# Performance work log

Measured on AMD Instinct MI355X. Metric: run time of the kernel, lower is better.

Reference implementation:

```python
import jax, jax.numpy as jnp
import numpy as np

N = 50000
E = 800000
IN_DIM = 256
HID = 64
HEADS = 4
OUT_DIM = 40
NEG_SLOPE = 0.2


def _gatv2_conv(x, src, dst, Wl, bl, Wr, br, att, bias, concat):
    """PyG GATv2Conv (share_weights=False, eval mode, no attn dropout).
    src -> message source nodes, dst -> target nodes (softmax over dst)."""
    H, C = att.shape
    n = x.shape[0]
    xl = (x @ Wl + bl).reshape(n, H, C)  # source/message transform (lin_l)
    xr = (x @ Wr + br).reshape(n, H, C)  # target transform (lin_r)
    # per-edge logits: [E, H]
    s = xl[src] + xr[dst]                                  # [E,H,C]
    e = jnp.einsum('ehc,hc->eh', jax.nn.leaky_relu(s, NEG_SLOPE), att)
    # segment softmax over incoming edges of each target node
    m = jax.ops.segment_max(e, dst, num_segments=n)        # [N,H]
    m = jnp.where(jnp.isfinite(m), m, 0.0)                 # empty segments
    ex = jnp.exp(e - m[dst])
    denom = jax.ops.segment_sum(ex, dst, num_segments=n)   # [N,H]
    alpha = ex / (denom[dst] + 1e-16)                      # [E,H]
    out = jax.ops.segment_sum(alpha[:, :, None] * xl[src], dst, num_segments=n)
    if concat:
        out = out.reshape(n, H * C)
    else:
        out = out.mean(axis=1)
    return out + bias


def setup_inputs() -> dict:
    key = jax.random.key(0)
    ks = jax.random.split(key, 12)
    sc = 0.05
    return {
        'x': jax.random.normal(ks[0], (N, IN_DIM), jnp.float32),
        'src': jax.random.randint(ks[1], (E,), 0, N, jnp.int32),
        'dst': jax.random.randint(ks[2], (E,), 0, N, jnp.int32),
        'Wl1': jax.random.normal(ks[3], (IN_DIM, HEADS * HID), jnp.float32) * sc,
        'bl1': jnp.zeros((HEADS * HID,), jnp.float32),
        'Wr1': jax.random.normal(ks[4], (IN_DIM, HEADS * HID), jnp.float32) * sc,
        'br1': jnp.zeros((HEADS * HID,), jnp.float32),
        'att1': jax.random.normal(ks[5], (HEADS, HID), jnp.float32) * sc,
        'bias1': jnp.zeros((HEADS * HID,), jnp.float32),
        'Wl2': jax.random.normal(ks[6], (HEADS * HID, HEADS * HID), jnp.float32) * sc,
        'bl2': jnp.zeros((HEADS * HID,), jnp.float32),
        'Wr2': jax.random.normal(ks[7], (HEADS * HID, HEADS * HID), jnp.float32) * sc,
        'br2': jnp.zeros((HEADS * HID,), jnp.float32),
        'att2': jax.random.normal(ks[8], (HEADS, HID), jnp.float32) * sc,
        'bias2': jnp.zeros((HID,), jnp.float32),
        'Wc': jax.random.normal(ks[9], (HID, OUT_DIM), jnp.float32) * sc,
        'bc': jnp.zeros((OUT_DIM,), jnp.float32),
    }


def reference(x, src, dst, Wl1, bl1, Wr1, br1, att1, bias1,
              Wl2, bl2, Wr2, br2, att2, bias2, Wc, bc):
    h = _gatv2_conv(x, src, dst, Wl1, bl1, Wr1, br1, att1, bias1, concat=True)
    h = jax.nn.relu(h)  # dropout p applied only in training; eval -> identity
    h = _gatv2_conv(h, src, dst, Wl2, bl2, Wr2, br2, att2, bias2, concat=False)
    h = jax.nn.relu(h)
    return h @ Wc + bc  # [N, OUT_DIM]
```

## Files before the change

### kernel.cpp

```cpp
#include <hip/hip_runtime.h>
#include <hip/hip_bf16.h>
#include <math.h>


#define IN_DIM 256
#define HIDHC 256
#define HID 64
#define OUT_DIM 40

using half8  = __attribute__((ext_vector_type(8))) _Float16;
using half4  = __attribute__((ext_vector_type(4))) _Float16;
using half2v = __attribute__((ext_vector_type(2))) _Float16;
using f32x4  = __attribute__((ext_vector_type(4))) float;

__device__ __forceinline__ void gload16(const void* g, void* l) {
    __builtin_amdgcn_global_load_lds(
        (const __attribute__((address_space(1))) void*)g,
        (__attribute__((address_space(3))) void*)l, 16, 0, 0);
}

__global__ void hist_prep(const int* __restrict__ dst, int* __restrict__ deg,
                          int* __restrict__ rank, int E, int nbh,
                          const float* __restrict__ x, _Float16* __restrict__ Af,
                          const float* __restrict__ W0, const float* __restrict__ W1,
                          const float* __restrict__ W2, const float* __restrict__ W3,
                          _Float16* __restrict__ T, int n4, int nb_cvt) {
    int bid = blockIdx.x;
    if (bid < nbh) {
        int i = bid * 256 + threadIdx.x;
        if (i < E) rank[i] = atomicAdd(&deg[dst[i]], 1);
    } else if (bid < nbh + nb_cvt) {
        int i = (bid - nbh) * 256 + threadIdx.x;
        if (i >= n4) return;
        float4 v = ((const float4*)x)[i];
        half4 h = { (_Float16)v.x, (_Float16)v.y, (_Float16)v.z, (_Float16)v.w };
        int node = i >> 6;
        int kb = (i & 63) * 4;
        size_t a = (size_t)(node >> 7) * 32768 + (size_t)(kb >> 3) * 1024
                 + (size_t)(node & 127) * 8 + (kb & 7);
        *(half4*)(Af + a) = h;
    } else {
        int widx = bid - nbh - nb_cvt;
        int wsel = widx >> 8, k = widx & 255, nn = threadIdx.x;
        const float* Wsel = (wsel == 0) ? W0 : (wsel == 1) ? W1
                          : (wsel == 2) ? W2 : W3;
        float v = Wsel[k * 256 + nn];
        size_t a = (size_t)wsel * 65536
                 + (size_t)(nn >> 7) * 32768 + (size_t)(k >> 5) * 4096
                 + (size_t)((k >> 3) & 3) * 1024 + (size_t)(nn & 127) * 8 + (k & 7);
        T[a] = (_Float16)v;
    }
}

__global__ void deg_block_reduce(const int* __restrict__ deg, int* __restrict__ bsum, int n) {
    int i = blockIdx.x * 256 + threadIdx.x;
    int v = (i < n) ? deg[i] : 0;
    #pragma unroll
    for (int off = 32; off; off >>= 1) v += __shfl_xor(v, off, 64);
    __shared__ int ws[4];
    int lane = threadIdx.x & 63, wid = threadIdx.x >> 6;
    if (lane == 0) ws[wid] = v;
    __syncthreads();
    if (threadIdx.x == 0) bsum[blockIdx.x] = ws[0] + ws[1] + ws[2] + ws[3];
}

__global__ void deg_scan_apply(const int* __restrict__ deg, const int* __restrict__ bsum,
                               int* __restrict__ offsets, int n, int nb) {
    int tid = threadIdx.x;
    int lane = tid & 63, wid = tid >> 6;

    __shared__ int pws[4];
    __shared__ int sadd;
    int pv = (tid < nb && tid < (int)blockIdx.x) ? bsum[tid] : 0;
    #pragma unroll
    for (int off = 32; off; off >>= 1) pv += __shfl_xor(pv, off, 64);
    if (lane == 0) pws[wid] = pv;
    __syncthreads();
    if (tid == 0) sadd = pws[0] + pws[1] + pws[2] + pws[3];
    __syncthreads();

    int i = blockIdx.x * 256 + tid;
    int v = (i < n) ? deg[i] : 0;
    int inc = v;
    #pragma unroll
    for (int off = 1; off < 64; off <<= 1) {
        int t = __shfl_up(inc, off, 64);
        if (lane >= off) inc += t;
    }
    __shared__ int ws[4];
    if (lane == 63) ws[wid] = inc;
    __syncthreads();
    int add = sadd;
    for (int w = 0; w < wid; ++w) add += ws[w];
    int incl = inc + add;
    if (i < n) offsets[i + 1] = incl;
    if (i == 0) offsets[0] = 0;
}


__device__ __forceinline__ void gemm_tile(
    const _Float16* __restrict__ Apk,
    const _Float16* __restrict__ W0, const float* __restrict__ b0, _Float16* __restrict__ C0,
    const _Float16* __restrict__ W1, const float* __restrict__ b1, _Float16* __restrict__ C1,
    int M, int bx, int by, _Float16* sA, _Float16* sW)
{
    int tid = threadIdx.x;
    int bm = bx * 128;
    int bn = by * 128;

    int lane = tid & 63, w = tid >> 6;
    int z  = w >> 2, wq = w & 3;
    int r = lane & 15, q = lane >> 4;
    int m0 = (wq >> 1) * 64, n0 = (wq & 1) * 64;

    const _Float16* Abase = Apk + (size_t)bx * 32768;
    const _Float16* W0b   = W0  + (size_t)by * 32768;
    const _Float16* W1b   = W1  + (size_t)by * 32768;
    int go = tid * 8;

    f32x4 acc[4][4];
    #pragma unroll
    for (int i = 0; i < 4; ++i)
        #pragma unroll
        for (int j = 0; j < 4; ++j) acc[i][j] = (f32x4)0.f;

    gload16(Abase + go, sA + go);
    gload16(W0b + go, sW + go);
    gload16(W1b + go, sW + 4096 + go);
    __builtin_amdgcn_s_waitcnt(0);
    __syncthreads();

    #pragma unroll 1
    for (int kt = 0; kt < 8; ++kt) {
        int buf = kt & 1;
        if (kt < 7) {
            int k0 = (kt + 1) * 4096;
            gload16(Abase + k0 + go, sA + (buf ^ 1) * 4096 + go);
            gload16(W0b + k0 + go, sW + ((buf ^ 1) * 2 + 0) * 4096 + go);
            gload16(W1b + k0 + go, sW + ((buf ^ 1) * 2 + 1) * 4096 + go);
        }
        half8 a[4], b[4];
        #pragma unroll
        for (int i = 0; i < 4; ++i) {
            a[i] = *(const half8*)(sA + buf * 4096 + (q * 128 + m0 + i * 16 + r) * 8);
            b[i] = *(const half8*)(sW + (buf * 2 + z) * 4096 + (q * 128 + n0 + i * 16 + r) * 8);
        }
        #pragma unroll
        for (int i = 0; i < 4; ++i)
            #pragma unroll
            for (int j = 0; j < 4; ++j)
                acc[i][j] = __builtin_amdgcn_mfma_f32_16x16x32_f16(a[i], b[j], acc[i][j], 0, 0, 0);
        __builtin_amdgcn_s_waitcnt(0);
        __syncthreads();
    }

    const float* bias = z ? b1 : b0;
    _Float16*    C    = z ? C1 : C0;

    float bv[4];
    #pragma unroll
    for (int j = 0; j < 4; ++j) bv[j] = bias[bn + n0 + j * 16 + r];
    #pragma unroll
    for (int i = 0; i < 4; ++i) {
        #pragma unroll
        for (int reg = 0; reg < 4; ++reg) {
            int orow = bm + m0 + i * 16 + q * 4 + reg;
            if (orow < M) {
                #pragma unroll
                for (int j = 0; j < 4; ++j)
                    C[(size_t)orow * 256 + bn + n0 + j * 16 + r] =
                        (_Float16)(acc[i][j][reg] + bv[j]);
            }
        }
    }
}

__global__ __launch_bounds__(512) void gemm_dual(
    const _Float16* __restrict__ Apk,
    const _Float16* __restrict__ W0, const float* __restrict__ b0, _Float16* __restrict__ C0,
    const _Float16* __restrict__ W1, const float* __restrict__ b1, _Float16* __restrict__ C1,
    int M)
{
    __shared__ __align__(16) _Float16 sA[2 * 4096];
    __shared__ __align__(16) _Float16 sW[2 * 2 * 4096];
    gemm_tile(Apk, W0, b0, C0, W1, b1, C1, M, blockIdx.x, blockIdx.y, sA, sW);
}

__global__ __launch_bounds__(512) void gemm_scatter(
    const _Float16* __restrict__ Apk,
    const _Float16* __restrict__ W0, const float* __restrict__ b0, _Float16* __restrict__ C0,
    const _Float16* __restrict__ W1, const float* __restrict__ b1, _Float16* __restrict__ C1,
    int M, int nbs,
    const int* __restrict__ src, const int* __restrict__ dst,
    const int* __restrict__ rank, const int* __restrict__ offsets,
    int* __restrict__ csr_src, int E)
{
    __shared__ __align__(16) _Float16 sA[2 * 4096];
    __shared__ __align__(16) _Float16 sW[2 * 2 * 4096];
    if ((int)blockIdx.x < nbs) {
        int e = blockIdx.x * 512 + threadIdx.x;
        if (e < E) {
            int d = dst[e];
            csr_src[offsets[d] + rank[e]] = src[e];
        }
        return;
    }
    int g = blockIdx.x - nbs;
    gemm_tile(Apk, W0, b0, C0, W1, b1, C1, M, g >> 1, g & 1, sA, sW);
}


__global__ __launch_bounds__(256) void gat_node(
    const _Float16* __restrict__ xl, const _Float16* __restrict__ xr,
    const float* __restrict__ att, const float* __restrict__ bias,
    const int* __restrict__ offsets, const int* __restrict__ csr_src,
    void* __restrict__ out0, int n, int mode)
{
    int wid = threadIdx.x >> 6;
    int node = (blockIdx.x << 2) + wid;
    if (node >= n) return;
    int lane = threadIdx.x & 63;
    int H = lane >> 5;
    int p = lane & 31;

    const half2v c02 = { (_Float16)0.2f, (_Float16)0.2f };

    half8 xrh = *(const half8*)(xr + (size_t)node * HIDHC + p * 8);
    half2v xr01 = __builtin_shufflevector(xrh, xrh, 0, 1);
    half2v xr23 = __builtin_shufflevector(xrh, xrh, 2, 3);
    half2v xr45 = __builtin_shufflevector(xrh, xrh, 4, 5);
    half2v xr67 = __builtin_shufflevector(xrh, xrh, 6, 7);

    float4 af0 = *(const float4*)(att + p * 8);
    float4 af1 = *(const float4*)(att + p * 8 + 4);
    half2v at01 = { (_Float16)af0.x, (_Float16)af0.y };
    half2v at23 = { (_Float16)af0.z, (_Float16)af0.w };
    half2v at45 = { (_Float16)af1.x, (_Float16)af1.y };
    half2v at67 = { (_Float16)af1.z, (_Float16)af1.w };

    float acc[8];
    #pragma unroll
    for (int k = 0; k < 8; ++k) acc[k] = 0.f;
    float d = 0.f;

    auto edge_compute = [&](half8 h) {
        half2v h01 = __builtin_shufflevector(h, h, 0, 1);
        half2v h23 = __builtin_shufflevector(h, h, 2, 3);
        half2v h45 = __builtin_shufflevector(h, h, 4, 5);
        half2v h67 = __builtin_shufflevector(h, h, 6, 7);
        half2v s01 = h01 + xr01, s23 = h23 + xr23, s45 = h45 + xr45, s67 = h67 + xr67;
        half2v l01 = __builtin_elementwise_max(s01, s01 * c02);
        half2v l23 = __builtin_elementwise_max(s23, s23 * c02);
        half2v l45 = __builtin_elementwise_max(s45, s45 * c02);
        half2v l67 = __builtin_elementwise_max(s67, s67 * c02);
        float e = __builtin_amdgcn_fdot2(l01, at01, 0.f, false);
        e = __builtin_amdgcn_fdot2(l23, at23, e, false);
        e = __builtin_amdgcn_fdot2(l45, at45, e, false);
        e = __builtin_amdgcn_fdot2(l67, at67, e, false);
        e += __shfl_xor(e, 1);
        e += __shfl_xor(e, 2);
        e += __shfl_xor(e, 4);
        float pw = __expf(e);
        d += pw;
        #pragma unroll
        for (int k = 0; k < 8; ++k) acc[k] = fmaf(pw, (float)h[k], acc[k]);
    };

    int j0 = __builtin_amdgcn_readfirstlane(offsets[node]);
    int j1 = __builtin_amdgcn_readfirstlane(offsets[node + 1]);
    int deg = j1 - j0;

    int fast = min(deg, 64);
    int npf = fast >> 1;
    int idxv = 0;
    if (lane < fast) idxv = csr_src[j0 + lane];

    half8 hA, hB;
    if (npf > 0) { int s = __shfl(idxv, 0 + H, 64); hA = *(const half8*)(xl + (size_t)s * HIDHC + p * 8); }
    if (npf > 1) { int s = __shfl(idxv, 2 + H, 64); hB = *(const half8*)(xl + (size_t)s * HIDHC + p * 8); }
    int t = 0;
    for (; t + 4 <= npf; t += 2) {
        half8 ha = hA, hb = hB;
        { int s = __shfl(idxv, (t + 2) * 2 + H, 64); hA = *(const half8*)(xl + (size_t)s * HIDHC + p * 8); }
        { int s = __shfl(idxv, (t + 3) * 2 + H, 64); hB = *(const half8*)(xl + (size_t)s * HIDHC + p * 8); }
        edge_compute(ha);
        edge_compute(hb);
    }
    if (t + 2 <= npf) {
        half8 ha = hA, hb = hB;
        if (t + 2 < npf) { int s = __shfl(idxv, (t + 2) * 2 + H, 64); hA = *(const half8*)(xl + (size_t)s * HIDHC + p * 8); }
        edge_compute(ha);
        edge_compute(hb);
        t += 2;
    }
    if (t < npf) {
        edge_compute(hA);
    }

    int j = j0 + (npf << 1);
    for (; j + 2 <= j1; j += 2) {
        int s0 = __builtin_amdgcn_readfirstlane(csr_src[j]);
        int s1 = __builtin_amdgcn_readfirstlane(csr_src[j + 1]);
        int s = H ? s1 : s0;
        half8 h = *(const half8*)(xl + (size_t)s * HIDHC + p * 8);
        edge_compute(h);
    }
    if (j < j1) {
        int s0 = __builtin_amdgcn_readfirstlane(csr_src[j]);
        half8 h = *(const half8*)(xl + (size_t)s0 * HIDHC + p * 8);
        half2v h01 = __builtin_shufflevector(h, h, 0, 1);
        half2v h23 = __builtin_shufflevector(h, h, 2, 3);
        half2v h45 = __builtin_shufflevector(h, h, 4, 5);
        half2v h67 = __builtin_shufflevector(h, h, 6, 7);
        half2v s01 = h01 + xr01, s23 = h23 + xr23, s45 = h45 + xr45, s67 = h67 + xr67;
        half2v l01 = __builtin_elementwise_max(s01, s01 * c02);
        half2v l23 = __builtin_elementwise_max(s23, s23 * c02);
        half2v l45 = __builtin_elementwise_max(s45, s45 * c02);
        half2v l67 = __builtin_elementwise_max(s67, s67 * c02);
        float e = __builtin_amdgcn_fdot2(l01, at01, 0.f, false);
        e = __builtin_amdgcn_fdot2(l23, at23, e, false);
        e = __builtin_amdgcn_fdot2(l45, at45, e, false);
        e = __builtin_amdgcn_fdot2(l67, at67, e, false);
        e += __shfl_xor(e, 1);
        e += __shfl_xor(e, 2);
        e += __shfl_xor(e, 4);
        float pw = (H == 0) ? __expf(e) : 0.f;
        d += pw;
        #pragma unroll
        for (int k = 0; k < 8; ++k) acc[k] = fmaf(pw, (float)h[k], acc[k]);
    }

    d += __shfl_xor(d, 32);
    #pragma unroll
    for (int k = 0; k < 8; ++k) acc[k] += __shfl_xor(acc[k], 32);

    float inv = 1.f / (d + 1e-16f);
    float o[8];
    #pragma unroll
    for (int k = 0; k < 8; ++k) o[k] = acc[k] * inv;

    if (mode == 0) {
        if (H == 0) {
            float4 b0 = *(const float4*)(bias + p * 8);
            float4 b1 = *(const float4*)(bias + p * 8 + 4);
            float bb[8] = { b0.x, b0.y, b0.z, b0.w, b1.x, b1.y, b1.z, b1.w };
            half8 hh;
            #pragma unroll
            for (int k = 0; k < 8; ++k) hh[k] = (_Float16)fmaxf(o[k] + bb[k], 0.f);
            _Float16* dstp = (_Float16*)out0 + (size_t)(node >> 7) * 32768
                           + (size_t)p * 1024 + (size_t)(node & 127) * 8;
            *(half8*)dstp = hh;
        }
    } else {
        #pragma unroll
        for (int k = 0; k < 8; ++k) {
            o[k] += __shfl_xor(o[k], 8);
            o[k] += __shfl_xor(o[k], 16);
        }
        if (lane < 8) {
            float4 b0 = *(const float4*)(bias + p * 8);
            float4 b1 = *(const float4*)(bias + p * 8 + 4);
            float bb[8] = { b0.x, b0.y, b0.z, b0.w, b1.x, b1.y, b1.z, b1.w };
            float4 o0, o1;
            o0.x = fmaxf(o[0] * 0.25f + bb[0], 0.f);
            o0.y = fmaxf(o[1] * 0.25f + bb[1], 0.f);
            o0.z = fmaxf(o[2] * 0.25f + bb[2], 0.f);
            o0.w = fmaxf(o[3] * 0.25f + bb[3], 0.f);
            o1.x = fmaxf(o[4] * 0.25f + bb[4], 0.f);
            o1.y = fmaxf(o[5] * 0.25f + bb[5], 0.f);
            o1.z = fmaxf(o[6] * 0.25f + bb[6], 0.f);
            o1.w = fmaxf(o[7] * 0.25f + bb[7], 0.f);
            float* dstp = (float*)out0 + (size_t)node * HID + p * 8;
            *(float4*)dstp = o0;
            *(float4*)(dstp + 4) = o1;
        }
    }
}


__global__ __launch_bounds__(256) void final_linear(
    const float* __restrict__ h2, const float* __restrict__ Wc,
    const float* __restrict__ bc, float* __restrict__ out, int n)
{
    __shared__ float Ws[HID * OUT_DIM];
    __shared__ float bs[OUT_DIM];
    __shared__ float hs[64][HID + 1];

    for (int i = threadIdx.x; i < HID * OUT_DIM; i += 256) Ws[i] = Wc[i];
    if (threadIdx.x < OUT_DIM) bs[threadIdx.x] = bc[threadIdx.x];

    int n0 = blockIdx.x * 64;
    for (int i = threadIdx.x; i < 64 * HID; i += 256) {
        int r = i >> 6, c = i & 63;
        int node = n0 + r;
        hs[r][c] = (node < n) ? h2[(size_t)node * HID + c] : 0.f;
    }
    __syncthreads();

    for (int idx = threadIdx.x; idx < 64 * OUT_DIM; idx += 256) {
        int r = idx / OUT_DIM, o = idx % OUT_DIM;
        int node = n0 + r;
        if (node < n) {
            float s = bs[o];
            #pragma unroll
            for (int c = 0; c < HID; ++c) s = fmaf(hs[r][c], Ws[c * OUT_DIM + o], s);
            out[(size_t)node * OUT_DIM + o] = s;
        }
    }
}


extern "C" void kernel_launch(void* const* d_in, const int* in_sizes, int n_in,
                              void* d_out, int out_size, void* d_ws, size_t ws_size,
                              hipStream_t stream) {
    const int N = in_sizes[0] / IN_DIM;
    const int E = in_sizes[1];

    const float* x    = (const float*)d_in[0];
    const int*   src  = (const int*)d_in[1];
    const int*   dst  = (const int*)d_in[2];
    const float* Wl1  = (const float*)d_in[3];
    const float* bl1  = (const float*)d_in[4];
    const float* Wr1  = (const float*)d_in[5];
    const float* br1  = (const float*)d_in[6];
    const float* att1 = (const float*)d_in[7];
    const float* bias1= (const float*)d_in[8];
    const float* Wl2  = (const float*)d_in[9];
    const float* bl2  = (const float*)d_in[10];
    const float* Wr2  = (const float*)d_in[11];
    const float* br2  = (const float*)d_in[12];
    const float* att2 = (const float*)d_in[13];
    const float* bias2= (const float*)d_in[14];
    const float* Wc   = (const float*)d_in[15];
    const float* bc   = (const float*)d_in[16];

    char* ws = (char*)d_ws;
    size_t off = 0;
    const int NT = (N + 127) / 128;
    _Float16* xlh = (_Float16*)(ws + off); off += (size_t)N * HIDHC * 2;
    _Float16* xrh = (_Float16*)(ws + off); off += (size_t)N * HIDHC * 2;
    _Float16* Af  = (_Float16*)(ws + off); off += (size_t)NT * 32768 * 2;
    float*    h2  = (float*)(ws + off);    off += (size_t)N * HID * 4;
    _Float16* Wt  = (_Float16*)(ws + off); off += (size_t)4 * 65536 * 2;
    int* deg     = (int*)(ws + off); off += (size_t)N * 4;
    int* offsets = (int*)(ws + off); off += (size_t)(N + 1) * 4;
    int* rank    = (int*)(ws + off); off += (size_t)E * 4;
    int* csr     = (int*)(ws + off); off += (size_t)E * 4;
    int* bsum    = (int*)(ws + off); off += 256 * 4;

    const int NB = (N + 255) / 256;

    hipMemsetAsync(deg, 0, (size_t)N * 4, stream);
    if (N & 127)
        hipMemsetAsync(Af + (size_t)(NT - 1) * 32768, 0, 32768 * 2, stream);

    const int nbh = (E + 255) / 256;
    const int n4 = N * HIDHC / 4;
    const int nb_cvt = (n4 + 255) / 256;
    hist_prep<<<nbh + nb_cvt + 1024, 256, 0, stream>>>(
        dst, deg, rank, E, nbh, x, Af, Wl1, Wr1, Wl2, Wr2, Wt, n4, nb_cvt);

    deg_block_reduce<<<NB, 256, 0, stream>>>(deg, bsum, N);
    deg_scan_apply<<<NB, 256, 0, stream>>>(deg, bsum, offsets, N, NB);

    const int KW = 65536;
    const int nbs = (E + 511) / 512;
    gemm_scatter<<<nbs + 2 * NT, 512, 0, stream>>>(Af,
        Wt + 0 * KW, bl1, xlh,
        Wt + 1 * KW, br1, xrh, N, nbs,
        src, dst, rank, offsets, csr, E);

    gat_node<<<(N + 3) / 4, 256, 0, stream>>>(xlh, xrh, att1, bias1, offsets, csr,
                                              (void*)Af, N, 0);
    gemm_dual<<<dim3(NT, 2), 512, 0, stream>>>(Af,
        Wt + 2 * KW, bl2, xlh,
        Wt + 3 * KW, br2, xrh, N);
    gat_node<<<(N + 3) / 4, 256, 0, stream>>>(xlh, xrh, att2, bias2, offsets, csr,
                                              (void*)h2, N, 1);
    final_linear<<<(N + 63) / 64, 256, 0, stream>>>(h2, Wc, bc, (float*)d_out, N);
}
```

Baseline: 381.5 us.

## Replace CSR build with fixed 64-slot per-node edge buckets plus overflow list

Builds per-destination adjacency directly during the histogram pass by writing each source into a fixed 64-entry slot array indexed by the atomic rank, with a global overflow list for degrees above 64. This removes the two prefix-scan kernels and the separate scatter pass, so the layer-1 GEMM can run as a plain dual GEMM. The node kernel reads degree and slots directly and scans the whole overflow list for high-degree nodes. The trade-offs are a larger padded CSR buffer with sparser reads, and a linear overflow scan that is slow if many nodes exceed 64 edges. With average degree 16, such nodes should be rare.

After: 386.0 us. About the same (+1.2%).

```diff
diff --git a/kernel.cpp b/kernel.cpp
--- a/kernel.cpp
+++ b/kernel.cpp
@@ -19,16 +19,28 @@
         (__attribute__((address_space(3))) void*)l, 16, 0, 0);
 }
 
-__global__ void hist_prep(const int* __restrict__ dst, int* __restrict__ deg,
-                          int* __restrict__ rank, int E, int nbh,
-                          const float* __restrict__ x, _Float16* __restrict__ Af,
-                          const float* __restrict__ W0, const float* __restrict__ W1,
-                          const float* __restrict__ W2, const float* __restrict__ W3,
-                          _Float16* __restrict__ T, int n4, int nb_cvt) {
+__global__ void hist_csr_prep(const int* __restrict__ src, const int* __restrict__ dst,
+                              int* __restrict__ deg, int* __restrict__ csr,
+                              int* __restrict__ oflow_cnt, int* __restrict__ oflow,
+                              int E, int nbh,
+                              const float* __restrict__ x, _Float16* __restrict__ Af,
+                              const float* __restrict__ W0, const float* __restrict__ W1,
+                              const float* __restrict__ W2, const float* __restrict__ W3,
+                              _Float16* __restrict__ T, int n4, int nb_cvt) {
     int bid = blockIdx.x;
     if (bid < nbh) {
         int i = bid * 256 + threadIdx.x;
-        if (i < E) rank[i] = atomicAdd(&deg[dst[i]], 1);
+        if (i < E) {
+            int d = dst[i];
+            int r = atomicAdd(&deg[d], 1);
+            if (r < 64) {
+                csr[d * 64 + r] = src[i];
+            } else {
+                int q = atomicAdd(oflow_cnt, 1);
+                oflow[2 * q] = d;
+                oflow[2 * q + 1] = src[i];
+            }
+        }
     } else if (bid < nbh + nb_cvt) {
         int i = (bid - nbh) * 256 + threadIdx.x;
         if (i >= n4) return;
@@ -52,51 +64,6 @@
     }
 }
 
-__global__ void deg_block_reduce(const int* __restrict__ deg, int* __restrict__ bsum, int n) {
-    int i = blockIdx.x * 256 + threadIdx.x;
-    int v = (i < n) ? deg[i] : 0;
-    #pragma unroll
-    for (int off = 32; off; off >>= 1) v += __shfl_xor(v, off, 64);
-    __shared__ int ws[4];
-    int lane = threadIdx.x & 63, wid = threadIdx.x >> 6;
-    if (lane == 0) ws[wid] = v;
-    __syncthreads();
-    if (threadIdx.x == 0) bsum[blockIdx.x] = ws[0] + ws[1] + ws[2] + ws[3];
-}
-
-__global__ void deg_scan_apply(const int* __restrict__ deg, const int* __restrict__ bsum,
-                               int* __restrict__ offsets, int n, int nb) {
-    int tid = threadIdx.x;
-    int lane = tid & 63, wid = tid >> 6;
-
-    __shared__ int pws[4];
-    __shared__ int sadd;
-    int pv = (tid < nb && tid < (int)blockIdx.x) ? bsum[tid] : 0;
-    #pragma unroll
-    for (int off = 32; off; off >>= 1) pv += __shfl_xor(pv, off, 64);
-    if (lane == 0) pws[wid] = pv;
-    __syncthreads();
-    if (tid == 0) sadd = pws[0] + pws[1] + pws[2] + pws[3];
-    __syncthreads();
-
-    int i = blockIdx.x * 256 + tid;
-    int v = (i < n) ? deg[i] : 0;
-    int inc = v;
-    #pragma unroll
-    for (int off = 1; off < 64; off <<= 1) {
-        int t = __shfl_up(inc, off, 64);
-        if (lane >= off) inc += t;
-    }
-    __shared__ int ws[4];
-    if (lane == 63) ws[wid] = inc;
-    __syncthreads();
-    int add = sadd;
-    for (int w = 0; w < wid; ++w) add += ws[w];
-    int incl = inc + add;
-    if (i < n) offsets[i + 1] = incl;
-    if (i == 0) offsets[0] = 0;
-}
-
 
 __device__ __forceinline__ void gemm_tile(
     const _Float16* __restrict__ Apk,
@@ -186,34 +153,12 @@
     gemm_tile(Apk, W0, b0, C0, W1, b1, C1, M, blockIdx.x, blockIdx.y, sA, sW);
 }
 
-__global__ __launch_bounds__(512) void gemm_scatter(
-    const _Float16* __restrict__ Apk,
-    const _Float16* __restrict__ W0, const float* __restrict__ b0, _Float16* __restrict__ C0,
-    const _Float16* __restrict__ W1, const float* __restrict__ b1, _Float16* __restrict__ C1,
-    int M, int nbs,
-    const int* __restrict__ src, const int* __restrict__ dst,
-    const int* __restrict__ rank, const int* __restrict__ offsets,
-    int* __restrict__ csr_src, int E)
-{
-    __shared__ __align__(16) _Float16 sA[2 * 4096];
-    __shared__ __align__(16) _Float16 sW[2 * 2 * 4096];
-    if ((int)blockIdx.x < nbs) {
-        int e = blockIdx.x * 512 + threadIdx.x;
-        if (e < E) {
-            int d = dst[e];
-            csr_src[offsets[d] + rank[e]] = src[e];
-        }
-        return;
-    }
-    int g = blockIdx.x - nbs;
-    gemm_tile(Apk, W0, b0, C0, W1, b1, C1, M, g >> 1, g & 1, sA, sW);
-}
-
 
 __global__ __launch_bounds__(256) void gat_node(
     const _Float16* __restrict__ xl, const _Float16* __restrict__ xr,
     const float* __restrict__ att, const float* __restrict__ bias,
-    const int* __restrict__ offsets, const int* __restrict__ csr_src,
+    const int* __restrict__ degv, const int* __restrict__ csr_src,
+    const int* __restrict__ oflow_cnt, const int* __restrict__ oflow,
     void* __restrict__ out0, int n, int mode)
 {
     int wid = threadIdx.x >> 6;
@@ -265,49 +210,7 @@
         #pragma unroll
         for (int k = 0; k < 8; ++k) acc[k] = fmaf(pw, (float)h[k], acc[k]);
     };
-
-    int j0 = __builtin_amdgcn_readfirstlane(offsets[node]);
-    int j1 = __builtin_amdgcn_readfirstlane(offsets[node + 1]);
-    int deg = j1 - j0;
-
-    int fast = min(deg, 64);
-    int npf = fast >> 1;
-    int idxv = 0;
-    if (lane < fast) idxv = csr_src[j0 + lane];
-
-    half8 hA, hB;
-    if (npf > 0) { int s = __shfl(idxv, 0 + H, 64); hA = *(const half8*)(xl + (size_t)s * HIDHC + p * 8); }
-    if (npf > 1) { int s = __shfl(idxv, 2 + H, 64); hB = *(const half8*)(xl + (size_t)s * HIDHC + p * 8); }
-    int t = 0;
-    for (; t + 4 <= npf; t += 2) {
-        half8 ha = hA, hb = hB;
-        { int s = __shfl(idxv, (t + 2) * 2 + H, 64); hA = *(const half8*)(xl + (size_t)s * HIDHC + p * 8); }
-        { int s = __shfl(idxv, (t + 3) * 2 + H, 64); hB = *(const half8*)(xl + (size_t)s * HIDHC + p * 8); }
-        edge_compute(ha);
-        edge_compute(hb);
-    }
-    if (t + 2 <= npf) {
-        half8 ha = hA, hb = hB;
-        if (t + 2 < npf) { int s = __shfl(idxv, (t + 2) * 2 + H, 64); hA = *(const half8*)(xl + (size_t)s * HIDHC + p * 8); }
-        edge_compute(ha);
-        edge_compute(hb);
-        t += 2;
-    }
-    if (t < npf) {
-        edge_compute(hA);
-    }
-
-    int j = j0 + (npf << 1);
-    for (; j + 2 <= j1; j += 2) {
-        int s0 = __builtin_amdgcn_readfirstlane(csr_src[j]);
-        int s1 = __builtin_amdgcn_readfirstlane(csr_src[j + 1]);
-        int s = H ? s1 : s0;
-        half8 h = *(const half8*)(xl + (size_t)s * HIDHC + p * 8);
-        edge_compute(h);
-    }
-    if (j < j1) {
-        int s0 = __builtin_amdgcn_readfirstlane(csr_src[j]);
-        half8 h = *(const half8*)(xl + (size_t)s0 * HIDHC + p * 8);
+    auto edge_compute_single = [&](half8 h) {
         half2v h01 = __builtin_shufflevector(h, h, 0, 1);
         half2v h23 = __builtin_shufflevector(h, h, 2, 3);
         half2v h45 = __builtin_shufflevector(h, h, 4, 5);
@@ -328,6 +231,53 @@
         d += pw;
         #pragma unroll
         for (int k = 0; k < 8; ++k) acc[k] = fmaf(pw, (float)h[k], acc[k]);
+    };
+
+    int dg = __builtin_amdgcn_readfirstlane(degv[node]);
+    int j0 = node << 6;
+
+    int fast = min(dg, 64);
+    int npf = fast >> 1;
+    int idxv = 0;
+    if (lane < fast) idxv = csr_src[j0 + lane];
+
+    half8 hA, hB;
+    if (npf > 0) { int s = __shfl(idxv, 0 + H, 64); hA = *(const half8*)(xl + (size_t)s * HIDHC + p * 8); }
+    if (npf > 1) { int s = __shfl(idxv, 2 + H, 64); hB = *(const half8*)(xl + (size_t)s * HIDHC + p * 8); }
+    int t = 0;
+    for (; t + 4 <= npf; t += 2) {
+        half8 ha = hA, hb = hB;
+        { int s = __shfl(idxv, (t + 2) * 2 + H, 64); hA = *(const half8*)(xl + (size_t)s * HIDHC + p * 8); }
+        { int s = __shfl(idxv, (t + 3) * 2 + H, 64); hB = *(const half8*)(xl + (size_t)s * HIDHC + p * 8); }
+        edge_compute(ha);
+        edge_compute(hb);
+    }
+    if (t + 2 <= npf) {
+        half8 ha = hA, hb = hB;
+        if (t + 2 < npf) { int s = __shfl(idxv, (t + 2) * 2 + H, 64); hA = *(const half8*)(xl + (size_t)s * HIDHC + p * 8); }
+        edge_compute(ha);
+        edge_compute(hb);
+        t += 2;
+    }
+    if (t < npf) {
+        edge_compute(hA);
+    }
+    if (fast & 1) {
+        int s0 = __shfl(idxv, fast - 1, 64);
+        half8 h = *(const half8*)(xl + (size_t)s0 * HIDHC + p * 8);
+        edge_compute_single(h);
+    }
+
+    if (dg > 64) {
+        int cnt = __builtin_amdgcn_readfirstlane(oflow_cnt[0]);
+        for (int k = 0; k < cnt; ++k) {
+            int dd = __builtin_amdgcn_readfirstlane(oflow[2 * k]);
+            if (dd == node) {
+                int ss = __builtin_amdgcn_readfirstlane(oflow[2 * k + 1]);
+                half8 h = *(const half8*)(xl + (size_t)ss * HIDHC + p * 8);
+                edge_compute_single(h);
+            }
+        }
     }
 
     d += __shfl_xor(d, 32);
@@ -442,40 +392,32 @@
     _Float16* Af  = (_Float16*)(ws + off); off += (size_t)NT * 32768 * 2;
     float*    h2  = (float*)(ws + off);    off += (size_t)N * HID * 4;
     _Float16* Wt  = (_Float16*)(ws + off); off += (size_t)4 * 65536 * 2;
-    int* deg     = (int*)(ws + off); off += (size_t)N * 4;
-    int* offsets = (int*)(ws + off); off += (size_t)(N + 1) * 4;
-    int* rank    = (int*)(ws + off); off += (size_t)E * 4;
-    int* csr     = (int*)(ws + off); off += (size_t)E * 4;
-    int* bsum    = (int*)(ws + off); off += 256 * 4;
-
-    const int NB = (N + 255) / 256;
-
-    hipMemsetAsync(deg, 0, (size_t)N * 4, stream);
+    int* deg      = (int*)(ws + off); off += (size_t)N * 4;
+    int* oflow_cnt= (int*)(ws + off); off += 4;
+    int* csr      = (int*)(ws + off); off += (size_t)N * 64 * 4;
+    int* oflow    = (int*)(ws + off); off += (size_t)E * 2 * 4;
+
+    hipMemsetAsync(deg, 0, ((size_t)N + 1) * 4, stream);
     if (N & 127)
         hipMemsetAsync(Af + (size_t)(NT - 1) * 32768, 0, 32768 * 2, stream);
 
     const int nbh = (E + 255) / 256;
     const int n4 = N * HIDHC / 4;
     const int nb_cvt = (n4 + 255) / 256;
-    hist_prep<<<nbh + nb_cvt + 1024, 256, 0, stream>>>(
-        dst, deg, rank, E, nbh, x, Af, Wl1, Wr1, Wl2, Wr2, Wt, n4, nb_cvt);
-
-    deg_block_reduce<<<NB, 256, 0, stream>>>(deg, bsum, N);
-    deg_scan_apply<<<NB, 256, 0, stream>>>(deg, bsum, offsets, N, NB);
+    hist_csr_prep<<<nbh + nb_cvt + 1024, 256, 0, stream>>>(
+        src, dst, deg, csr, oflow_cnt, oflow, E, nbh,
+        x, Af, Wl1, Wr1, Wl2, Wr2, Wt, n4, nb_cvt);
 
     const int KW = 65536;
-    const int nbs = (E + 511) / 512;
-    gemm_scatter<<<nbs + 2 * NT, 512, 0, stream>>>(Af,
+    gemm_dual<<<dim3(NT, 2), 512, 0, stream>>>(Af,
         Wt + 0 * KW, bl1, xlh,
-        Wt + 1 * KW, br1, xrh, N, nbs,
-        src, dst, rank, offsets, csr, E);
-
-    gat_node<<<(N + 3) / 4, 256, 0, stream>>>(xlh, xrh, att1, bias1, offsets, csr,
-                                              (void*)Af, N, 0);
+        Wt + 1 * KW, br1, xrh, N);
+    gat_node<<<(N + 3) / 4, 256, 0, stream>>>(xlh, xrh, att1, bias1, deg, csr,
+                                              oflow_cnt, oflow, (void*)Af, N, 0);
     gemm_dual<<<dim3(NT, 2), 512, 0, stream>>>(Af,
         Wt + 2 * KW, bl2, xlh,
         Wt + 3 * KW, br2, xrh, N);
-    gat_node<<<(N + 3) / 4, 256, 0, stream>>>(xlh, xrh, att2, bias2, offsets, csr,
-                                              (void*)h2, N, 1);
+    gat_node<<<(N + 3) / 4, 256, 0, stream>>>(xlh, xrh, att2, bias2, deg, csr,
+                                              oflow_cnt, oflow, (void*)h2, N, 1);
     final_linear<<<(N + 63) / 64, 256, 0, stream>>>(h2, Wc, bc, (float*)d_out, N);
 }
```
